# Optimization experiments

Measured on AMD Instinct MI355X. Metric: run time of the kernel, lower is better.

## Reference

```python
import jax, jax.numpy as jnp
import numpy as np

NUM_HEADS = 8
SCALE_BASE = 512.0
GN_EPS = 1e-5


def rotate_every_two(x):
    x1 = x[..., ::2]
    x2 = x[..., 1::2]
    return jnp.stack([-x2, x1], axis=-1).reshape(x.shape)


def xpos_apply(x, downscale):
    # x: [B, T, D]; XPOS rotary with length-dependent scale (offset=0)
    L, D = x.shape[1], x.shape[2]
    half = D // 2
    scale_vec = (jnp.arange(0, D, 2, dtype=jnp.float32) + 0.4 * D) / (1.4 * D)  # [half]
    pos = jnp.arange(L, dtype=jnp.float32)
    scale = scale_vec[None, :] ** (pos[:, None] / SCALE_BASE)  # [L, half]
    inv_freq = 1.0 / (10000.0 ** (jnp.arange(half, dtype=jnp.float32) / half))
    sinusoid = pos[:, None] * inv_freq[None, :]  # [L, half]
    sin, cos = jnp.sin(sinusoid), jnp.cos(sinusoid)
    if downscale:
        scale = 1.0 / scale
    sin_s = jnp.repeat(sin * scale, 2, axis=-1)  # duplicate_interleave -> [L, D]
    cos_s = jnp.repeat(cos * scale, 2, axis=-1)
    return x * cos_s + rotate_every_two(x) * sin_s


def decay_mask_fn(T, num_heads):
    # gamma per head; decay stored as log(gamma) so mask = gamma^(i-j) on lower triangle
    s, e = np.log(1.0 / 32.0), np.log(1.0 / 512.0)
    gamma = 1.0 - jnp.exp(jnp.linspace(s, e, num_heads).astype(jnp.float32))
    log_decay = jnp.log(gamma)  # [H], negative
    idx = jnp.arange(T)
    expo = (idx[:, None] - idx[None, :]).astype(jnp.float32)  # i - j
    tri = (idx[:, None] >= idx[None, :])
    expo_safe = jnp.where(tri, expo, 0.0)
    mask = jnp.exp(log_decay[:, None, None] * expo_safe) * tri  # [H, T, T]
    scale = jnp.sqrt(mask.sum(axis=-1, keepdims=True))  # [H, T, 1]
    return mask / scale


def setup_inputs() -> dict:
    key = jax.random.key(0)
    ks = jax.random.split(key, 4)
    B, T, E = 2, 2048, 1024
    V = 2 * E
    return {
        "hidden_states": jax.random.normal(ks[0], (B, T, E), dtype=jnp.float32),
        "w_qkv": jax.random.normal(ks[1], (E, 2 * E + V), dtype=jnp.float32) * 0.02,
        "b_qkv": jnp.zeros((2 * E + V,), dtype=jnp.float32),
        "w_g": jax.random.normal(ks[2], (E, V), dtype=jnp.float32) * 0.02,
        "b_g": jnp.zeros((V,), dtype=jnp.float32),
        "w_p": jax.random.normal(ks[3], (V, E), dtype=jnp.float32) * 0.02,
        "b_p": jnp.zeros((E,), dtype=jnp.float32),
    }


def reference(hidden_states, w_qkv, b_qkv, w_g, b_g, w_p, b_p):
    B, T, E = hidden_states.shape
    H = NUM_HEADS
    V = 2 * E
    dk, dv = E // H, V // H

    qkv = hidden_states @ w_qkv + b_qkv
    q, k, v = qkv[..., :E], qkv[..., E:2 * E], qkv[..., 2 * E:]
    q = xpos_apply(q, downscale=False)
    k = xpos_apply(k, downscale=True)

    # split heads -> [B, H, T, d]
    q = q.reshape(B, T, H, dk).transpose(0, 2, 1, 3)
    k = k.reshape(B, T, H, dk).transpose(0, 2, 1, 3)
    v = v.reshape(B, T, H, dv).transpose(0, 2, 1, 3)

    mask = decay_mask_fn(T, H)  # [H, T, T]

    # parallel retention
    retention = jnp.einsum("bhid,bhjd->bhij", q, k) * (dk ** -0.5)
    retention = retention * mask[None]  # [B, H, T, T]
    out = jnp.einsum("bhij,bhjv->bhiv", retention, v)

    # current_kv = sum_j mask[h, -1, j] * k_j (x) v_j
    curr_kv = jnp.einsum("hj,bhjk,bhjv->bhkv", mask[:, -1, :], k, v)

    retention_out = out.transpose(0, 2, 1, 3).reshape(B, T, V)

    # GroupNorm(num_groups=H, affine=False) over v_dim channels
    g = retention_out.reshape(B * T, H, dv)
    mu = g.mean(axis=-1, keepdims=True)
    var = ((g - mu) ** 2).mean(axis=-1, keepdims=True)
    normed = ((g - mu) / jnp.sqrt(var + GN_EPS)).reshape(B, T, V)

    gated = jax.nn.silu(hidden_states @ w_g + b_g) * normed
    proj = gated @ w_p + b_p
    return proj, curr_kv
```

## Files before the change

kernel.cpp:

```cpp
#include <hip/hip_runtime.h>
#include <math.h>

#define BT      4096
#define T_SEQ   2048
#define E_DIM   1024
#define V_DIM   2048
#define DK      128
#define DV      256

typedef unsigned short ushort_t;
typedef __attribute__((ext_vector_type(8)))  short bf16x8;
typedef __attribute__((ext_vector_type(4)))  unsigned short u16x4;
typedef __attribute__((ext_vector_type(16))) float f32x16;

__device__ __forceinline__ void decay_params(int h, float& ld, float& gamma) {
    const float s0 = -3.4657359027997265f;
    const float e0 = -6.2383246250395092f;
    float lin = s0 + (e0 - s0) * ((float)h * (1.0f / 7.0f));
    gamma = 1.0f - expf(lin);
    ld = logf(gamma);
}

__device__ __forceinline__ short f2bf(float f) {
    unsigned u = __float_as_uint(f);
    unsigned r = (u + 0x7fffu + ((u >> 16) & 1u)) >> 16;
    return (short)r;
}
__device__ __forceinline__ float bf2f(ushort_t u) {
    return __uint_as_float((unsigned)u << 16);
}

__device__ __forceinline__ void async_copy16(void* lds, const void* g) {
    __builtin_amdgcn_global_load_lds(
        (const __attribute__((address_space(1))) unsigned int*)g,
        (__attribute__((address_space(3))) unsigned int*)lds, 16, 0, 0);
}

__device__ __forceinline__ void xcd_tile(int& bx, int& by) {
    const int nwgx = gridDim.x;
    const int nwg  = nwgx * gridDim.y;
    int bid = blockIdx.y * nwgx + blockIdx.x;
    bid = (bid & 7) * (nwg >> 3) + (bid >> 3);
    bx = bid % nwgx;
    by = bid / nwgx;
}

__device__ __forceinline__ void xcd_map_qkv(int& bx, int& by) {
    int bid = blockIdx.y * 16 + blockIdx.x;
    const int xcd = bid & 7, idx = bid >> 3;
    bx = (xcd & 1) * 8 + (idx & 7);
    by = (xcd >> 1) * 4 + (idx >> 3);
}

__device__ __forceinline__ void xcd_map_gate(int& bx, int& by) {
    int bid = blockIdx.y * 8 + blockIdx.x;
    const int xcd = bid & 7, idx = bid >> 3;
    bx = (xcd & 1) * 4 + (idx & 3);
    by = (xcd >> 1) * 8 + (idx >> 2);
}

__global__ __launch_bounds__(256)
void f32_to_bf16_kernel(const float* __restrict__ in, ushort_t* __restrict__ out)
{
    int i = (blockIdx.x * 256 + threadIdx.x) * 8;
    float4 a = *(const float4*)&in[i];
    float4 b = *(const float4*)&in[i + 4];
    bf16x8 o;
    o[0] = f2bf(a.x); o[1] = f2bf(a.y); o[2] = f2bf(a.z); o[3] = f2bf(a.w);
    o[4] = f2bf(b.x); o[5] = f2bf(b.y); o[6] = f2bf(b.z); o[7] = f2bf(b.w);
    *(bf16x8*)&out[i] = o;
}

__global__ __launch_bounds__(256)
void transpose_w_kernel(const float* __restrict__ W, ushort_t* __restrict__ Wt,
                        int K, int N)
{
    __shared__ float tile[32][33];
    const int k0 = blockIdx.y * 32, n0 = blockIdx.x * 32;
    const int t = threadIdx.x;
    const int r = t >> 3, c = (t & 7) * 4;
    float4 v = *(const float4*)&W[(size_t)(k0 + r) * N + n0 + c];
    tile[r][c] = v.x; tile[r][c + 1] = v.y; tile[r][c + 2] = v.z; tile[r][c + 3] = v.w;
    __syncthreads();
    u16x4 o;
    o[0] = (ushort_t)f2bf(tile[c][r]);
    o[1] = (ushort_t)f2bf(tile[c + 1][r]);
    o[2] = (ushort_t)f2bf(tile[c + 2][r]);
    o[3] = (ushort_t)f2bf(tile[c + 3][r]);
    *(u16x4*)&Wt[(size_t)(n0 + r) * K + k0 + c] = o;
}

__global__ __launch_bounds__(512, 2)
void gemm256p8(const ushort_t* __restrict__ A,
               const ushort_t* __restrict__ Bt,
               const float* __restrict__ bias,
               ushort_t* __restrict__ C, int ldc, int nkt)
{
    __shared__ ushort_t As[2 * 16384];
    __shared__ ushort_t Bs[2 * 16384];

    const int tid = threadIdx.x;
    const int wid = tid >> 6, l = tid & 63;
    const int lc = l & 31, q = l >> 5;
    const int wr = wid >> 2, wc = wid & 3;
    int bx, by; xcd_map_qkv(bx, by);
    const int m0 = by * 256, n0 = bx * 256;

    const int sra = tid >> 3;
    const int spa = (tid & 7) ^ (sra & 7);
    const ushort_t* gA = A + (size_t)(m0 + sra) * 1024 + spa * 8;
    const int srb = tid >> 2;
    const int spb = (tid & 3) ^ ((srb >> 1) & 3);
    const ushort_t* gB = Bt + (size_t)(n0 + srb) * 1024 + spb * 8;
    const int da = tid * 8;

    int arow0 = (wr * 128 +  0 + lc) * 64;
    int arow1 = (wr * 128 + 32 + lc) * 64;
    int arow2 = (wr * 128 + 64 + lc) * 64;
    int arow3 = (wr * 128 + 96 + lc) * 64;
    int sk0 = ((0 * 2 + q) ^ (lc & 7)) * 8;
    int sk1 = ((1 * 2 + q) ^ (lc & 7)) * 8;
    int sk2 = ((2 * 2 + q) ^ (lc & 7)) * 8;
    int sk3 = ((3 * 2 + q) ^ (lc & 7)) * 8;
    int brow0 = (wc * 64 +  0 + lc) * 32;
    int brow1 = (wc * 64 + 32 + lc) * 32;
    int tk0 = ((0 + q) ^ ((lc >> 1) & 3)) * 8;
    int tk1 = ((2 + q) ^ ((lc >> 1) & 3)) * 8;
    int tk2 = 8192 + ((0 + q) ^ ((lc >> 1) & 3)) * 8;
    int tk3 = 8192 + ((2 + q) ^ ((lc >> 1) & 3)) * 8;

    f32x16 acc[4][2];
    #pragma unroll
    for (int mi = 0; mi < 4; ++mi)
        #pragma unroll
        for (int ni = 0; ni < 2; ++ni)
            #pragma unroll
            for (int e = 0; e < 16; ++e) acc[mi][ni][e] = 0.0f;

    async_copy16(&As[da],          gA);
    async_copy16(&As[8192 + da],   gA + 131072);
    async_copy16(&Bs[da],          gB);
    async_copy16(&Bs[4096 + da],   gB + 131072);
    async_copy16(&As[4096 + da],   gA + 65536);
    async_copy16(&As[12288 + da],  gA + 196608);
    async_copy16(&Bs[8192 + da],   gB + 32);
    async_copy16(&Bs[12288 + da],  gB + 131072 + 32);
    gA += 64; gB += 64;
    asm volatile("s_waitcnt vmcnt(0)" ::: "memory");
    __builtin_amdgcn_s_barrier();

    int cur = 0;
    for (int t = 0; t < nkt - 1; ++t) {
        const int cb = cur * 16384;
        const int nb = 16384 - cb;
        bf16x8 a00 = *(const bf16x8*)&As[cb + arow0 + sk0];
        bf16x8 a01 = *(const bf16x8*)&As[cb + arow0 + sk1];
        bf16x8 a10 = *(const bf16x8*)&As[cb + arow1 + sk0];
        bf16x8 a11 = *(const bf16x8*)&As[cb + arow1 + sk1];
        bf16x8 b00 = *(const bf16x8*)&Bs[cb + brow0 + tk0];
        bf16x8 b01 = *(const bf16x8*)&Bs[cb + brow0 + tk1];
        bf16x8 b10 = *(const bf16x8*)&Bs[cb + brow1 + tk0];
        bf16x8 b11 = *(const bf16x8*)&Bs[cb + brow1 + tk1];
        async_copy16(&As[nb + da],        gA);
        async_copy16(&As[nb + 8192 + da], gA + 131072);
        async_copy16(&Bs[nb + da],        gB);
        async_copy16(&Bs[nb + 4096 + da], gB + 131072);
        __builtin_amdgcn_s_barrier();
        asm volatile("s_waitcnt lgkmcnt(0)" ::: "memory");
        __builtin_amdgcn_s_setprio(1);
        acc[0][0] = __builtin_amdgcn_mfma_f32_32x32x16_bf16(a00, b00, acc[0][0], 0, 0, 0);
        acc[0][1] = __builtin_amdgcn_mfma_f32_32x32x16_bf16(a00, b10, acc[0][1], 0, 0, 0);
        acc[1][0] = __builtin_amdgcn_mfma_f32_32x32x16_bf16(a10, b00, acc[1][0], 0, 0, 0);
        acc[1][1] = __builtin_amdgcn_mfma_f32_32x32x16_bf16(a10, b10, acc[1][1], 0, 0, 0);
        acc[0][0] = __builtin_amdgcn_mfma_f32_32x32x16_bf16(a01, b01, acc[0][0], 0, 0, 0);
        acc[0][1] = __builtin_amdgcn_mfma_f32_32x32x16_bf16(a01, b11, acc[0][1], 0, 0, 0);
        acc[1][0] = __builtin_amdgcn_mfma_f32_32x32x16_bf16(a11, b01, acc[1][0], 0, 0, 0);
        acc[1][1] = __builtin_amdgcn_mfma_f32_32x32x16_bf16(a11, b11, acc[1][1], 0, 0, 0);
        __builtin_amdgcn_s_setprio(0);
        asm volatile("s_waitcnt vmcnt(6)" ::: "memory");
        __builtin_amdgcn_s_barrier();
        bf16x8 a20 = *(const bf16x8*)&As[cb + arow2 + sk0];
        bf16x8 a21 = *(const bf16x8*)&As[cb + arow2 + sk1];
        bf16x8 a30 = *(const bf16x8*)&As[cb + arow3 + sk0];
        bf16x8 a31 = *(const bf16x8*)&As[cb + arow3 + sk1];
        async_copy16(&As[nb + 4096 + da],  gA + 65536);
        async_copy16(&As[nb + 12288 + da], gA + 196608);
        __builtin_amdgcn_s_barrier();
        asm volatile("s_waitcnt lgkmcnt(0)" ::: "memory");
        __builtin_amdgcn_s_setprio(1);
        acc[2][0] = __builtin_amdgcn_mfma_f32_32x32x16_bf16(a20, b00, acc[2][0], 0, 0, 0);
        acc[2][1] = __builtin_amdgcn_mfma_f32_32x32x16_bf16(a20, b10, acc[2][1], 0, 0, 0);
        acc[3][0] = __builtin_amdgcn_mfma_f32_32x32x16_bf16(a30, b00, acc[3][0], 0, 0, 0);
        acc[3][1] = __builtin_amdgcn_mfma_f32_32x32x16_bf16(a30, b10, acc[3][1], 0, 0, 0);
        acc[2][0] = __builtin_amdgcn_mfma_f32_32x32x16_bf16(a21, b01, acc[2][0], 0, 0, 0);
        acc[2][1] = __builtin_amdgcn_mfma_f32_32x32x16_bf16(a21, b11, acc[2][1], 0, 0, 0);
        acc[3][0] = __builtin_amdgcn_mfma_f32_32x32x16_bf16(a31, b01, acc[3][0], 0, 0, 0);
        acc[3][1] = __builtin_amdgcn_mfma_f32_32x32x16_bf16(a31, b11, acc[3][1], 0, 0, 0);
        __builtin_amdgcn_s_setprio(0);
        asm volatile("s_waitcnt vmcnt(6)" ::: "memory");
        __builtin_amdgcn_s_barrier();
        bf16x8 a02 = *(const bf16x8*)&As[cb + arow0 + sk2];
        bf16x8 a03 = *(const bf16x8*)&As[cb + arow0 + sk3];
        bf16x8 a12 = *(const bf16x8*)&As[cb + arow1 + sk2];
        bf16x8 a13 = *(const bf16x8*)&As[cb + arow1 + sk3];
        bf16x8 b02 = *(const bf16x8*)&Bs[cb + brow0 + tk2];
        bf16x8 b03 = *(const bf16x8*)&Bs[cb + brow0 + tk3];
        bf16x8 b12 = *(const bf16x8*)&Bs[cb + brow1 + tk2];
        bf16x8 b13 = *(const bf16x8*)&Bs[cb + brow1 + tk3];
        async_copy16(&Bs[nb + 8192 + da],  gB + 32);
        async_copy16(&Bs[nb + 12288 + da], gB + 131072 + 32);
        gA += 64; gB += 64;
        __builtin_amdgcn_s_barrier();
        asm volatile("s_waitcnt lgkmcnt(0)" ::: "memory");
        __builtin_amdgcn_s_setprio(1);
        acc[0][0] = __builtin_amdgcn_mfma_f32_32x32x16_bf16(a02, b02, acc[0][0], 0, 0, 0);
        acc[0][1] = __builtin_amdgcn_mfma_f32_32x32x16_bf16(a02, b12, acc[0][1], 0, 0, 0);
        acc[1][0] = __builtin_amdgcn_mfma_f32_32x32x16_bf16(a12, b02, acc[1][0], 0, 0, 0);
        acc[1][1] = __builtin_amdgcn_mfma_f32_32x32x16_bf16(a12, b12, acc[1][1], 0, 0, 0);
        acc[0][0] = __builtin_amdgcn_mfma_f32_32x32x16_bf16(a03, b03, acc[0][0], 0, 0, 0);
        acc[0][1] = __builtin_amdgcn_mfma_f32_32x32x16_bf16(a03, b13, acc[0][1], 0, 0, 0);
        acc[1][0] = __builtin_amdgcn_mfma_f32_32x32x16_bf16(a13, b03, acc[1][0], 0, 0, 0);
        acc[1][1] = __builtin_amdgcn_mfma_f32_32x32x16_bf16(a13, b13, acc[1][1], 0, 0, 0);
        __builtin_amdgcn_s_setprio(0);
        __builtin_amdgcn_s_barrier();
        bf16x8 a22 = *(const bf16x8*)&As[cb + arow2 + sk2];
        bf16x8 a23 = *(const bf16x8*)&As[cb + arow2 + sk3];
        bf16x8 a32 = *(const bf16x8*)&As[cb + arow3 + sk2];
        bf16x8 a33 = *(const bf16x8*)&As[cb + arow3 + sk3];
        __builtin_amdgcn_s_barrier();
        asm volatile("s_waitcnt lgkmcnt(0)" ::: "memory");
        __builtin_amdgcn_s_setprio(1);
        acc[2][0] = __builtin_amdgcn_mfma_f32_32x32x16_bf16(a22, b02, acc[2][0], 0, 0, 0);
        acc[2][1] = __builtin_amdgcn_mfma_f32_32x32x16_bf16(a22, b12, acc[2][1], 0, 0, 0);
        acc[3][0] = __builtin_amdgcn_mfma_f32_32x32x16_bf16(a32, b02, acc[3][0], 0, 0, 0);
        acc[3][1] = __builtin_amdgcn_mfma_f32_32x32x16_bf16(a32, b12, acc[3][1], 0, 0, 0);
        acc[2][0] = __builtin_amdgcn_mfma_f32_32x32x16_bf16(a23, b03, acc[2][0], 0, 0, 0);
        acc[2][1] = __builtin_amdgcn_mfma_f32_32x32x16_bf16(a23, b13, acc[2][1], 0, 0, 0);
        acc[3][0] = __builtin_amdgcn_mfma_f32_32x32x16_bf16(a33, b03, acc[3][0], 0, 0, 0);
        acc[3][1] = __builtin_amdgcn_mfma_f32_32x32x16_bf16(a33, b13, acc[3][1], 0, 0, 0);
        __builtin_amdgcn_s_setprio(0);
        asm volatile("s_waitcnt vmcnt(4)" ::: "memory");
        __builtin_amdgcn_s_barrier();
        cur ^= 1;
    }

    {
        const int cb = cur * 16384;
        bf16x8 a00 = *(const bf16x8*)&As[cb + arow0 + sk0];
        bf16x8 a01 = *(const bf16x8*)&As[cb + arow0 + sk1];
        bf16x8 a10 = *(const bf16x8*)&As[cb + arow1 + sk0];
        bf16x8 a11 = *(const bf16x8*)&As[cb + arow1 + sk1];
        bf16x8 b00 = *(const bf16x8*)&Bs[cb + brow0 + tk0];
        bf16x8 b01 = *(const bf16x8*)&Bs[cb + brow0 + tk1];
        bf16x8 b10 = *(const bf16x8*)&Bs[cb + brow1 + tk0];
        bf16x8 b11 = *(const bf16x8*)&Bs[cb + brow1 + tk1];
        __builtin_amdgcn_s_barrier();
        asm volatile("s_waitcnt lgkmcnt(0)" ::: "memory");
        __builtin_amdgcn_s_setprio(1);
        acc[0][0] = __builtin_amdgcn_mfma_f32_32x32x16_bf16(a00, b00, acc[0][0], 0, 0, 0);
        acc[0][1] = __builtin_amdgcn_mfma_f32_32x32x16_bf16(a00, b10, acc[0][1], 0, 0, 0);
        acc[1][0] = __builtin_amdgcn_mfma_f32_32x32x16_bf16(a10, b00, acc[1][0], 0, 0, 0);
        acc[1][1] = __builtin_amdgcn_mfma_f32_32x32x16_bf16(a10, b10, acc[1][1], 0, 0, 0);
        acc[0][0] = __builtin_amdgcn_mfma_f32_32x32x16_bf16(a01, b01, acc[0][0], 0, 0, 0);
        acc[0][1] = __builtin_amdgcn_mfma_f32_32x32x16_bf16(a01, b11, acc[0][1], 0, 0, 0);
        acc[1][0] = __builtin_amdgcn_mfma_f32_32x32x16_bf16(a11, b01, acc[1][0], 0, 0, 0);
        acc[1][1] = __builtin_amdgcn_mfma_f32_32x32x16_bf16(a11, b11, acc[1][1], 0, 0, 0);
        __builtin_amdgcn_s_setprio(0);
        asm volatile("s_waitcnt vmcnt(2)" ::: "memory");
        __builtin_amdgcn_s_barrier();
        bf16x8 a20 = *(const bf16x8*)&As[cb + arow2 + sk0];
        bf16x8 a21 = *(const bf16x8*)&As[cb + arow2 + sk1];
        bf16x8 a30 = *(const bf16x8*)&As[cb + arow3 + sk0];
        bf16x8 a31 = *(const bf16x8*)&As[cb + arow3 + sk1];
        __builtin_amdgcn_s_barrier();
        asm volatile("s_waitcnt lgkmcnt(0)" ::: "memory");
        __builtin_amdgcn_s_setprio(1);
        acc[2][0] = __builtin_amdgcn_mfma_f32_32x32x16_bf16(a20, b00, acc[2][0], 0, 0, 0);
        acc[2][1] = __builtin_amdgcn_mfma_f32_32x32x16_bf16(a20, b10, acc[2][1], 0, 0, 0);
        acc[3][0] = __builtin_amdgcn_mfma_f32_32x32x16_bf16(a30, b00, acc[3][0], 0, 0, 0);
        acc[3][1] = __builtin_amdgcn_mfma_f32_32x32x16_bf16(a30, b10, acc[3][1], 0, 0, 0);
        acc[2][0] = __builtin_amdgcn_mfma_f32_32x32x16_bf16(a21, b01, acc[2][0], 0, 0, 0);
        acc[2][1] = __builtin_amdgcn_mfma_f32_32x32x16_bf16(a21, b11, acc[2][1], 0, 0, 0);
        acc[3][0] = __builtin_amdgcn_mfma_f32_32x32x16_bf16(a31, b01, acc[3][0], 0, 0, 0);
        acc[3][1] = __builtin_amdgcn_mfma_f32_32x32x16_bf16(a31, b11, acc[3][1], 0, 0, 0);
        __builtin_amdgcn_s_setprio(0);
        asm volatile("s_waitcnt vmcnt(0)" ::: "memory");
        __builtin_amdgcn_s_barrier();
        bf16x8 a02 = *(const bf16x8*)&As[cb + arow0 + sk2];
        bf16x8 a03 = *(const bf16x8*)&As[cb + arow0 + sk3];
        bf16x8 a12 = *(const bf16x8*)&As[cb + arow1 + sk2];
        bf16x8 a13 = *(const bf16x8*)&As[cb + arow1 + sk3];
        bf16x8 b02 = *(const bf16x8*)&Bs[cb + brow0 + tk2];
        bf16x8 b03 = *(const bf16x8*)&Bs[cb + brow0 + tk3];
        bf16x8 b12 = *(const bf16x8*)&Bs[cb + brow1 + tk2];
        bf16x8 b13 = *(const bf16x8*)&Bs[cb + brow1 + tk3];
        __builtin_amdgcn_s_barrier();
        asm volatile("s_waitcnt lgkmcnt(0)" ::: "memory");
        __builtin_amdgcn_s_setprio(1);
        acc[0][0] = __builtin_amdgcn_mfma_f32_32x32x16_bf16(a02, b02, acc[0][0], 0, 0, 0);
        acc[0][1] = __builtin_amdgcn_mfma_f32_32x32x16_bf16(a02, b12, acc[0][1], 0, 0, 0);
        acc[1][0] = __builtin_amdgcn_mfma_f32_32x32x16_bf16(a12, b02, acc[1][0], 0, 0, 0);
        acc[1][1] = __builtin_amdgcn_mfma_f32_32x32x16_bf16(a12, b12, acc[1][1], 0, 0, 0);
        acc[0][0] = __builtin_amdgcn_mfma_f32_32x32x16_bf16(a03, b03, acc[0][0], 0, 0, 0);
        acc[0][1] = __builtin_amdgcn_mfma_f32_32x32x16_bf16(a03, b13, acc[0][1], 0, 0, 0);
        acc[1][0] = __builtin_amdgcn_mfma_f32_32x32x16_bf16(a13, b03, acc[1][0], 0, 0, 0);
        acc[1][1] = __builtin_amdgcn_mfma_f32_32x32x16_bf16(a13, b13, acc[1][1], 0, 0, 0);
        __builtin_amdgcn_s_setprio(0);
        __builtin_amdgcn_s_barrier();
        bf16x8 a22 = *(const bf16x8*)&As[cb + arow2 + sk2];
        bf16x8 a23 = *(const bf16x8*)&As[cb + arow2 + sk3];
        bf16x8 a32 = *(const bf16x8*)&As[cb + arow3 + sk2];
        bf16x8 a33 = *(const bf16x8*)&As[cb + arow3 + sk3];
        asm volatile("s_waitcnt lgkmcnt(0)" ::: "memory");
        __builtin_amdgcn_s_setprio(1);
        acc[2][0] = __builtin_amdgcn_mfma_f32_32x32x16_bf16(a22, b02, acc[2][0], 0, 0, 0);
        acc[2][1] = __builtin_amdgcn_mfma_f32_32x32x16_bf16(a22, b12, acc[2][1], 0, 0, 0);
        acc[3][0] = __builtin_amdgcn_mfma_f32_32x32x16_bf16(a32, b02, acc[3][0], 0, 0, 0);
        acc[3][1] = __builtin_amdgcn_mfma_f32_32x32x16_bf16(a32, b12, acc[3][1], 0, 0, 0);
        acc[2][0] = __builtin_amdgcn_mfma_f32_32x32x16_bf16(a23, b03, acc[2][0], 0, 0, 0);
        acc[2][1] = __builtin_amdgcn_mfma_f32_32x32x16_bf16(a23, b13, acc[2][1], 0, 0, 0);
        acc[3][0] = __builtin_amdgcn_mfma_f32_32x32x16_bf16(a33, b03, acc[3][0], 0, 0, 0);
        acc[3][1] = __builtin_amdgcn_mfma_f32_32x32x16_bf16(a33, b13, acc[3][1], 0, 0, 0);
        __builtin_amdgcn_s_setprio(0);
    }

    {
        const float bb0 = bias[n0 + wc * 64 + lc];
        const float bb1 = bias[n0 + wc * 64 + 32 + lc];
        #pragma unroll
        for (int mi = 0; mi < 4; ++mi) {
            #pragma unroll
            for (int r = 0; r < 16; ++r) {
                const int row = m0 + wr * 128 + mi * 32 + (r & 3) + 8 * (r >> 2) + 4 * q;
                ushort_t* cp = C + (size_t)row * ldc + n0 + wc * 64 + lc;
                cp[0]  = (ushort_t)f2bf(acc[mi][0][r] + bb0);
                cp[32] = (ushort_t)f2bf(acc[mi][1][r] + bb1);
            }
        }
    }
}

__global__ __launch_bounds__(512)
void gemm_gate_p8(const ushort_t* __restrict__ A,
                  const ushort_t* __restrict__ Bt,
                  const float* __restrict__ bias,
                  ushort_t* __restrict__ C, int ldc,
                  int nkt)
{
    __shared__ ushort_t As[2 * 8192];
    __shared__ ushort_t Bs[2 * 16384];

    const int tid = threadIdx.x;
    const int wid = tid >> 6, l = tid & 63;
    const int lc = l & 31, q = l >> 5;
    const int wr = wid >> 2, wc = wid & 3;
    int bx, by; xcd_map_gate(bx, by);
    const int m0 = by * 128, n0 = bx * 256;

    const int sra = tid >> 3;
    const int spa = (tid & 7) ^ (sra & 7);
    const ushort_t* gA = A + (size_t)(m0 + sra) * 1024 + spa * 8;
    const int srb = tid >> 2;
    const int spb = (tid & 3) ^ ((srb >> 1) & 3);
    const ushort_t* gB = Bt + (size_t)(n0 + srb) * 1024 + spb * 8;
    const int da = tid * 8;

    int arow0 = (wr * 64 +  0 + lc) * 64;
    int arow1 = (wr * 64 + 32 + lc) * 64;
    int sk0 = ((0 * 2 + q) ^ (lc & 7)) * 8;
    int sk1 = ((1 * 2 + q) ^ (lc & 7)) * 8;
    int sk2 = ((2 * 2 + q) ^ (lc & 7)) * 8;
    int sk3 = ((3 * 2 + q) ^ (lc & 7)) * 8;
    int brow0 = (wc * 64 +  0 + lc) * 32;
    int brow1 = (wc * 64 + 32 + lc) * 32;
    int tk0 = ((0 + q) ^ ((lc >> 1) & 3)) * 8;
    int tk1 = ((2 + q) ^ ((lc >> 1) & 3)) * 8;
    int tk2 = 8192 + ((0 + q) ^ ((lc >> 1) & 3)) * 8;
    int tk3 = 8192 + ((2 + q) ^ ((lc >> 1) & 3)) * 8;

    f32x16 acc[2][2];
    #pragma unroll
    for (int mi = 0; mi < 2; ++mi)
        #pragma unroll
        for (int ni = 0; ni < 2; ++ni)
            #pragma unroll
            for (int e = 0; e < 16; ++e) acc[mi][ni][e] = 0.0f;

    async_copy16(&As[da],          gA);
    async_copy16(&As[4096 + da],   gA + 65536);
    async_copy16(&Bs[da],          gB);
    async_copy16(&Bs[4096 + da],   gB + 131072);
    async_copy16(&Bs[8192 + da],   gB + 32);
    async_copy16(&Bs[12288 + da],  gB + 131072 + 32);
    gA += 64; gB += 64;
    asm volatile("s_waitcnt vmcnt(0)" ::: "memory");
    __builtin_amdgcn_s_barrier();

    int cur = 0;
    for (int t = 0; t < nkt - 1; ++t) {
        const int ca = cur * 8192,  na = 8192 - ca;
        const int cb = cur * 16384, nb = 16384 - cb;
        bf16x8 a00 = *(const bf16x8*)&As[ca + arow0 + sk0];
        bf16x8 a01 = *(const bf16x8*)&As[ca + arow0 + sk1];
        bf16x8 a10 = *(const bf16x8*)&As[ca + arow1 + sk0];
        bf16x8 a11 = *(const bf16x8*)&As[ca + arow1 + sk1];
        bf16x8 b00 = *(const bf16x8*)&Bs[cb + brow0 + tk0];
        bf16x8 b01 = *(const bf16x8*)&Bs[cb + brow0 + tk1];
        bf16x8 b10 = *(const bf16x8*)&Bs[cb + brow1 + tk0];
        bf16x8 b11 = *(const bf16x8*)&Bs[cb + brow1 + tk1];
        async_copy16(&As[na + da],        gA);
        async_copy16(&As[na + 4096 + da], gA + 65536);
        async_copy16(&Bs[nb + da],        gB);
        async_copy16(&Bs[nb + 4096 + da], gB + 131072);
        __builtin_amdgcn_s_barrier();
        asm volatile("s_waitcnt lgkmcnt(0)" ::: "memory");
        __builtin_amdgcn_s_setprio(1);
        acc[0][0] = __builtin_amdgcn_mfma_f32_32x32x16_bf16(a00, b00, acc[0][0], 0, 0, 0);
// ... 442 lines not shown
            pa1[e]     = f2bf(q ? t3 : sv[e + 8]);
            pa1[e + 4] = f2bf(q ? sv[e + 12] : t2);
        }

        #pragma unroll
        for (int vg = 0; vg < 8; ++vg) {
            const ushort_t* vp = vt + ((size_t)bh * 256 + vg * 32 + lc) * T_SEQ + j0 + q * 8;
            bf16x8 vb0 = *(const bf16x8*)vp;
            bf16x8 vb1 = *(const bf16x8*)(vp + 16);
            acc[vg] = __builtin_amdgcn_mfma_f32_32x32x16_bf16(pa0, vb0, acc[vg], 0, 0, 0);
            acc[vg] = __builtin_amdgcn_mfma_f32_32x32x16_bf16(pa1, vb1, acc[vg], 0, 0, 0);
        }
    }

    #pragma unroll
    for (int r = 0; r < 16; ++r) {
        const int il = (r & 3) + 8 * (r >> 2) + 4 * q;
        const int i  = i0 + il;
        float denom = (1.0f - expf(ld * (float)(i + 1))) / (1.0f - gamma);
        float fs = 0.08838834764831845f * rsqrtf(denom);
        float vals[8];
        float a1 = 0.0f, a2 = 0.0f;
        #pragma unroll
        for (int vg = 0; vg < 8; ++vg) {
            float x = acc[vg][r] * fs;
            vals[vg] = x;
            a1 += x; a2 += x * x;
        }
        a1 += __shfl_xor(a1, 1);  a2 += __shfl_xor(a2, 1);
        a1 += __shfl_xor(a1, 2);  a2 += __shfl_xor(a2, 2);
        a1 += __shfl_xor(a1, 4);  a2 += __shfl_xor(a2, 4);
        a1 += __shfl_xor(a1, 8);  a2 += __shfl_xor(a2, 8);
        a1 += __shfl_xor(a1, 16); a2 += __shfl_xor(a2, 16);
        float mu = a1 * (1.0f / 256.0f);
        float var = a2 * (1.0f / 256.0f) - mu * mu;
        float rs = rsqrtf(var + 1e-5f);
        const size_t ob = ((size_t)(b * T_SEQ + i)) * V_DIM + h * DV + lc;
        ushort_t* op = gated + ob;
        const ushort_t* gp = grw + ob;
        #pragma unroll
        for (int vg = 0; vg < 8; ++vg) {
            float g = bf2f(gp[vg * 32]);
            op[vg * 32] = (ushort_t)f2bf((vals[vg] - mu) * rs * g);
        }
    }
}

extern "C" void kernel_launch(void* const* d_in, const int* in_sizes, int n_in,
                              void* d_out, int out_size, void* d_ws, size_t ws_size,
                              hipStream_t stream)
{
    const float* hs    = (const float*)d_in[0];
    const float* w_qkv = (const float*)d_in[1];
    const float* b_qkv = (const float*)d_in[2];
    const float* w_g   = (const float*)d_in[3];
    const float* b_g   = (const float*)d_in[4];
    const float* w_p   = (const float*)d_in[5];
    const float* b_p   = (const float*)d_in[6];
    float* out = (float*)d_out;

    const size_t MB = 1024 * 1024;
    ushort_t* qkv_bf   = (ushort_t*)d_ws;
    ushort_t* Abuf     = (ushort_t*)d_ws;
    ushort_t* Stbuf    = (ushort_t*)d_ws;
    ushort_t* wp_t     = (ushort_t*)d_ws;
    ushort_t* gate_raw = (ushort_t*)((char*)d_ws + 32 * MB);
    ushort_t* gated_bf = (ushort_t*)((char*)d_ws + 48 * MB);
    ushort_t* wg_t     = (ushort_t*)((char*)d_ws + 64 * MB);
    ushort_t* qh       = (ushort_t*)((char*)d_ws + 64 * MB);
    ushort_t* vt       = (ushort_t*)((char*)d_ws + 72 * MB);
    ushort_t* wqkv_t   = (ushort_t*)((char*)d_ws + 88 * MB);
    ushort_t* kh       = (ushort_t*)((char*)d_ws + 88 * MB);
    ushort_t* hs_bf    = (ushort_t*)d_out;
    ushort_t* kt2      = (ushort_t*)((char*)d_out + 8 * MB);
    float*    ckv_out  = out + (size_t)BT * E_DIM;

    f32_to_bf16_kernel<<<dim3(2048), 256, 0, stream>>>(hs, hs_bf);
    transpose_w_kernel<<<dim3(64, 32), 256, 0, stream>>>(w_g, wg_t, E_DIM, V_DIM);
    transpose_w_kernel<<<dim3(128, 32), 256, 0, stream>>>(w_qkv, wqkv_t, E_DIM, 4096);

    gemm_gate_p8<<<dim3(8, 32), 512, 0, stream>>>(
        hs_bf, wg_t, b_g, gate_raw, V_DIM, E_DIM / 64);

    gemm256p8<<<dim3(16, 16), 512, 0, stream>>>(
        hs_bf, wqkv_t, b_qkv, qkv_bf, 4096, E_DIM / 64);

    qk_prep<<<dim3(BT), 256, 0, stream>>>(qkv_bf, qh, kh);
    v_transpose<<<dim3(64, 128), 256, 0, stream>>>(qkv_bf, vt);
    kt2_kernel<<<dim3(64, 64), 256, 0, stream>>>(kh, kt2);

    chunk_kv<<<dim3(32, 16), 256, 0, stream>>>(vt, kt2, Abuf);
    scan_state<<<dim3(2048), 256, 0, stream>>>(Abuf, Stbuf, ckv_out);
    retention_chunk<<<dim3(64, 16), 64, 0, stream>>>(qh, kh, vt, Stbuf, gate_raw, gated_bf);

    transpose_w_kernel<<<dim3(32, 64), 256, 0, stream>>>(w_p, wp_t, V_DIM, E_DIM);
    gemm_tm64<<<dim3(8, 64), 256, 0, stream>>>(
        gated_bf, V_DIM, wp_t, V_DIM, b_p, out, E_DIM, V_DIM / 32);
}
```

Before: 297.4 us.

## Rewrite QKV GEMM as 256x128 tile with 3-stage BK=32 LDS pipeline

```diff
diff --git a/kernel.cpp b/kernel.cpp
--- a/kernel.cpp
+++ b/kernel.cpp
@@ -45,11 +45,11 @@
     by = bid / nwgx;
 }
 
-__device__ __forceinline__ void xcd_map_qkv(int& bx, int& by) {
-    int bid = blockIdx.y * 16 + blockIdx.x;
+__device__ __forceinline__ void xcd_map_qkv2(int& bx, int& by) {
+    int bid = blockIdx.y * 32 + blockIdx.x;
     const int xcd = bid & 7, idx = bid >> 3;
-    bx = (xcd & 1) * 8 + (idx & 7);
-    by = (xcd >> 1) * 4 + (idx >> 3);
+    bx = (xcd & 3) * 8 + (idx & 7);
+    by = (xcd >> 2) * 8 + (idx >> 3);
 }
 
 __device__ __forceinline__ void xcd_map_gate(int& bx, int& by) {
@@ -90,44 +90,40 @@
     *(u16x4*)&Wt[(size_t)(n0 + r) * K + k0 + c] = o;
 }
 
-__global__ __launch_bounds__(512, 2)
-void gemm256p8(const ushort_t* __restrict__ A,
-               const ushort_t* __restrict__ Bt,
-               const float* __restrict__ bias,
-               ushort_t* __restrict__ C, int ldc, int nkt)
-{
-    __shared__ ushort_t As[2 * 16384];
-    __shared__ ushort_t Bs[2 * 16384];
+__global__ __launch_bounds__(256, 2)
+void gemm_qkv_v2(const ushort_t* __restrict__ A,
+                 const ushort_t* __restrict__ Bt,
+                 const float* __restrict__ bias,
+                 ushort_t* __restrict__ C, int ldc, int nkt)
+{
+    __shared__ ushort_t As[3 * 8192];
+    __shared__ ushort_t Bs[3 * 4096];
 
     const int tid = threadIdx.x;
-    const int wid = tid >> 6, l = tid & 63;
+    const int w  = tid >> 6, l = tid & 63;
     const int lc = l & 31, q = l >> 5;
-    const int wr = wid >> 2, wc = wid & 3;
-    int bx, by; xcd_map_qkv(bx, by);
-    const int m0 = by * 256, n0 = bx * 256;
-
-    const int sra = tid >> 3;
-    const int spa = (tid & 7) ^ (sra & 7);
-    const ushort_t* gA = A + (size_t)(m0 + sra) * 1024 + spa * 8;
-    const int srb = tid >> 2;
-    const int spb = (tid & 3) ^ ((srb >> 1) & 3);
-    const ushort_t* gB = Bt + (size_t)(n0 + srb) * 1024 + spb * 8;
-    const int da = tid * 8;
-
-    int arow0 = (wr * 128 +  0 + lc) * 64;
-    int arow1 = (wr * 128 + 32 + lc) * 64;
-    int arow2 = (wr * 128 + 64 + lc) * 64;
-    int arow3 = (wr * 128 + 96 + lc) * 64;
-    int sk0 = ((0 * 2 + q) ^ (lc & 7)) * 8;
-    int sk1 = ((1 * 2 + q) ^ (lc & 7)) * 8;
-    int sk2 = ((2 * 2 + q) ^ (lc & 7)) * 8;
-    int sk3 = ((3 * 2 + q) ^ (lc & 7)) * 8;
-    int brow0 = (wc * 64 +  0 + lc) * 32;
-    int brow1 = (wc * 64 + 32 + lc) * 32;
-    int tk0 = ((0 + q) ^ ((lc >> 1) & 3)) * 8;
-    int tk1 = ((2 + q) ^ ((lc >> 1) & 3)) * 8;
-    int tk2 = 8192 + ((0 + q) ^ ((lc >> 1) & 3)) * 8;
-    int tk3 = 8192 + ((2 + q) ^ ((lc >> 1) & 3)) * 8;
+    const int wr = w >> 1, wcn = w & 1;
+    int bx, by; xcd_map_qkv2(bx, by);
+    const int m0 = by * 256, n0 = bx * 128;
+
+    const int rb = tid >> 2;
+    const int kc = (tid & 3) ^ ((rb >> 1) & 3);
+    const ushort_t* gA = A  + (size_t)(m0 + rb) * 1024 + kc * 8;
+    const ushort_t* gB = Bt + (size_t)(n0 + rb) * 1024 + kc * 8;
+    const int dst = tid * 8;
+
+    const int sl = (lc >> 1) & 3;
+    int aoff[4][2], boff[2][2];
+    #pragma unroll
+    for (int ks = 0; ks < 2; ++ks) {
+        const int kk = ks * 2 + q;
+        #pragma unroll
+        for (int mi = 0; mi < 4; ++mi)
+            aoff[mi][ks] = ((wr * 128 + mi * 32 + lc) * 4 + (kk ^ sl)) * 8;
+        #pragma unroll
+        for (int ni = 0; ni < 2; ++ni)
+            boff[ni][ks] = ((wcn * 64 + ni * 32 + lc) * 4 + (kk ^ sl)) * 8;
+    }
 
     f32x16 acc[4][2];
     #pragma unroll
@@ -137,34 +133,36 @@
             #pragma unroll
             for (int e = 0; e < 16; ++e) acc[mi][ni][e] = 0.0f;
 
-    async_copy16(&As[da],          gA);
-    async_copy16(&As[8192 + da],   gA + 131072);
-    async_copy16(&Bs[da],          gB);
-    async_copy16(&Bs[4096 + da],   gB + 131072);
-    async_copy16(&As[4096 + da],   gA + 65536);
-    async_copy16(&As[12288 + da],  gA + 196608);
-    async_copy16(&Bs[8192 + da],   gB + 32);
-    async_copy16(&Bs[12288 + da],  gB + 131072 + 32);
-    gA += 64; gB += 64;
-    asm volatile("s_waitcnt vmcnt(0)" ::: "memory");
+    auto stageA = [&](int ab) {
+        async_copy16(&As[ab + 0 * 2048 + dst], gA + 0 * 65536);
+        async_copy16(&As[ab + 1 * 2048 + dst], gA + 1 * 65536);
+        async_copy16(&As[ab + 2 * 2048 + dst], gA + 2 * 65536);
+        async_copy16(&As[ab + 3 * 2048 + dst], gA + 3 * 65536);
+        gA += 32;
+    };
+    auto stageB = [&](int bb) {
+        async_copy16(&Bs[bb + 0 * 2048 + dst], gB + 0 * 65536);
+        async_copy16(&Bs[bb + 1 * 2048 + dst], gB + 1 * 65536);
+        gB += 32;
+    };
+
+    stageA(0);     stageB(0);
+    stageA(8192);  stageB(4096);
+    asm volatile("s_waitcnt vmcnt(6)" ::: "memory");
     __builtin_amdgcn_s_barrier();
 
-    int cur = 0;
-    for (int t = 0; t < nkt - 1; ++t) {
-        const int cb = cur * 16384;
-        const int nb = 16384 - cb;
-        bf16x8 a00 = *(const bf16x8*)&As[cb + arow0 + sk0];
-        bf16x8 a01 = *(const bf16x8*)&As[cb + arow0 + sk1];
-        bf16x8 a10 = *(const bf16x8*)&As[cb + arow1 + sk0];
-        bf16x8 a11 = *(const bf16x8*)&As[cb + arow1 + sk1];
-        bf16x8 b00 = *(const bf16x8*)&Bs[cb + brow0 + tk0];
-        bf16x8 b01 = *(const bf16x8*)&Bs[cb + brow0 + tk1];
-        bf16x8 b10 = *(const bf16x8*)&Bs[cb + brow1 + tk0];
-        bf16x8 b11 = *(const bf16x8*)&Bs[cb + brow1 + tk1];
-        async_copy16(&As[nb + da],        gA);
-        async_copy16(&As[nb + 8192 + da], gA + 131072);
-        async_copy16(&Bs[nb + da],        gB);
-        async_copy16(&Bs[nb + 4096 + da], gB + 131072);
+    int as_ = 16384, bs_ = 8192;
+    int ac_ = 0,     bc_ = 0;
+    for (int t = 0; t < nkt - 2; ++t) {
+        bf16x8 b00 = *(const bf16x8*)&Bs[bc_ + boff[0][0]];
+        bf16x8 b01 = *(const bf16x8*)&Bs[bc_ + boff[0][1]];
+        bf16x8 b10 = *(const bf16x8*)&Bs[bc_ + boff[1][0]];
+        bf16x8 b11 = *(const bf16x8*)&Bs[bc_ + boff[1][1]];
+        bf16x8 a00 = *(const bf16x8*)&As[ac_ + aoff[0][0]];
+        bf16x8 a01 = *(const bf16x8*)&As[ac_ + aoff[0][1]];
+        bf16x8 a10 = *(const bf16x8*)&As[ac_ + aoff[1][0]];
+        bf16x8 a11 = *(const bf16x8*)&As[ac_ + aoff[1][1]];
+        stageA(as_);
         __builtin_amdgcn_s_barrier();
         asm volatile("s_waitcnt lgkmcnt(0)" ::: "memory");
         __builtin_amdgcn_s_setprio(1);
@@ -177,14 +175,12 @@
         acc[1][0] = __builtin_amdgcn_mfma_f32_32x32x16_bf16(a11, b01, acc[1][0], 0, 0, 0);
         acc[1][1] = __builtin_amdgcn_mfma_f32_32x32x16_bf16(a11, b11, acc[1][1], 0, 0, 0);
         __builtin_amdgcn_s_setprio(0);
-        asm volatile("s_waitcnt vmcnt(6)" ::: "memory");
-        __builtin_amdgcn_s_barrier();
-        bf16x8 a20 = *(const bf16x8*)&As[cb + arow2 + sk0];
-        bf16x8 a21 = *(const bf16x8*)&As[cb + arow2 + sk1];
-        bf16x8 a30 = *(const bf16x8*)&As[cb + arow3 + sk0];
-        bf16x8 a31 = *(const bf16x8*)&As[cb + arow3 + sk1];
-        async_copy16(&As[nb + 4096 + da],  gA + 65536);
-        async_copy16(&As[nb + 12288 + da], gA + 196608);
+        __builtin_amdgcn_s_barrier();
+        bf16x8 a20 = *(const bf16x8*)&As[ac_ + aoff[2][0]];
+        bf16x8 a21 = *(const bf16x8*)&As[ac_ + aoff[2][1]];
+        bf16x8 a30 = *(const bf16x8*)&As[ac_ + aoff[3][0]];
+        bf16x8 a31 = *(const bf16x8*)&As[ac_ + aoff[3][1]];
+        stageB(bs_);
         __builtin_amdgcn_s_barrier();
         asm volatile("s_waitcnt lgkmcnt(0)" ::: "memory");
         __builtin_amdgcn_s_setprio(1);
@@ -199,140 +195,64 @@
         __builtin_amdgcn_s_setprio(0);
         asm volatile("s_waitcnt vmcnt(6)" ::: "memory");
         __builtin_amdgcn_s_barrier();
-        bf16x8 a02 = *(const bf16x8*)&As[cb + arow0 + sk2];
-        bf16x8 a03 = *(const bf16x8*)&As[cb + arow0 + sk3];
-        bf16x8 a12 = *(const bf16x8*)&As[cb + arow1 + sk2];
-        bf16x8 a13 = *(const bf16x8*)&As[cb + arow1 + sk3];
-        bf16x8 b02 = *(const bf16x8*)&Bs[cb + brow0 + tk2];
-        bf16x8 b03 = *(const bf16x8*)&Bs[cb + brow0 + tk3];
-        bf16x8 b12 = *(const bf16x8*)&Bs[cb + brow1 + tk2];
-        bf16x8 b13 = *(const bf16x8*)&Bs[cb + brow1 + tk3];
-        async_copy16(&Bs[nb + 8192 + da],  gB + 32);
-        async_copy16(&Bs[nb + 12288 + da], gB + 131072 + 32);
-        gA += 64; gB += 64;
-        __builtin_amdgcn_s_barrier();
-        asm volatile("s_waitcnt lgkmcnt(0)" ::: "memory");
-        __builtin_amdgcn_s_setprio(1);
-        acc[0][0] = __builtin_amdgcn_mfma_f32_32x32x16_bf16(a02, b02, acc[0][0], 0, 0, 0);
-        acc[0][1] = __builtin_amdgcn_mfma_f32_32x32x16_bf16(a02, b12, acc[0][1], 0, 0, 0);
-        acc[1][0] = __builtin_amdgcn_mfma_f32_32x32x16_bf16(a12, b02, acc[1][0], 0, 0, 0);
-        acc[1][1] = __builtin_amdgcn_mfma_f32_32x32x16_bf16(a12, b12, acc[1][1], 0, 0, 0);
-        acc[0][0] = __builtin_amdgcn_mfma_f32_32x32x16_bf16(a03, b03, acc[0][0], 0, 0, 0);
-        acc[0][1] = __builtin_amdgcn_mfma_f32_32x32x16_bf16(a03, b13, acc[0][1], 0, 0, 0);
-        acc[1][0] = __builtin_amdgcn_mfma_f32_32x32x16_bf16(a13, b03, acc[1][0], 0, 0, 0);
-        acc[1][1] = __builtin_amdgcn_mfma_f32_32x32x16_bf16(a13, b13, acc[1][1], 0, 0, 0);
-        __builtin_amdgcn_s_setprio(0);
-        __builtin_amdgcn_s_barrier();
-        bf16x8 a22 = *(const bf16x8*)&As[cb + arow2 + sk2];
-        bf16x8 a23 = *(const bf16x8*)&As[cb + arow2 + sk3];
-        bf16x8 a32 = *(const bf16x8*)&As[cb + arow3 + sk2];
-        bf16x8 a33 = *(const bf16x8*)&As[cb + arow3 + sk3];
-        __builtin_amdgcn_s_barrier();
-        asm volatile("s_waitcnt lgkmcnt(0)" ::: "memory");
-        __builtin_amdgcn_s_setprio(1);
-        acc[2][0] = __builtin_amdgcn_mfma_f32_32x32x16_bf16(a22, b02, acc[2][0], 0, 0, 0);
-        acc[2][1] = __builtin_amdgcn_mfma_f32_32x32x16_bf16(a22, b12, acc[2][1], 0, 0, 0);
-        acc[3][0] = __builtin_amdgcn_mfma_f32_32x32x16_bf16(a32, b02, acc[3][0], 0, 0, 0);
-        acc[3][1] = __builtin_amdgcn_mfma_f32_32x32x16_bf16(a32, b12, acc[3][1], 0, 0, 0);
-        acc[2][0] = __builtin_amdgcn_mfma_f32_32x32x16_bf16(a23, b03, acc[2][0], 0, 0, 0);
-        acc[2][1] = __builtin_amdgcn_mfma_f32_32x32x16_bf16(a23, b13, acc[2][1], 0, 0, 0);
-        acc[3][0] = __builtin_amdgcn_mfma_f32_32x32x16_bf16(a33, b03, acc[3][0], 0, 0, 0);
-        acc[3][1] = __builtin_amdgcn_mfma_f32_32x32x16_bf16(a33, b13, acc[3][1], 0, 0, 0);
-        __builtin_amdgcn_s_setprio(0);
-        asm volatile("s_waitcnt vmcnt(4)" ::: "memory");
-        __builtin_amdgcn_s_barrier();
-        cur ^= 1;
+        as_ = ac_; bs_ = bc_;
+        ac_ = (ac_ == 16384) ? 0 : ac_ + 8192;
+        bc_ = (bc_ == 8192)  ? 0 : bc_ + 4096;
     }
 
     {
-        const int cb = cur * 16384;
-        bf16x8 a00 = *(const bf16x8*)&As[cb + arow0 + sk0];
-        bf16x8 a01 = *(const bf16x8*)&As[cb + arow0 + sk1];
-        bf16x8 a10 = *(const bf16x8*)&As[cb + arow1 + sk0];
-        bf16x8 a11 = *(const bf16x8*)&As[cb + arow1 + sk1];
-        bf16x8 b00 = *(const bf16x8*)&Bs[cb + brow0 + tk0];
-        bf16x8 b01 = *(const bf16x8*)&Bs[cb + brow0 + tk1];
-        bf16x8 b10 = *(const bf16x8*)&Bs[cb + brow1 + tk0];
-        bf16x8 b11 = *(const bf16x8*)&Bs[cb + brow1 + tk1];
-        __builtin_amdgcn_s_barrier();
-        asm volatile("s_waitcnt lgkmcnt(0)" ::: "memory");
-        __builtin_amdgcn_s_setprio(1);
-        acc[0][0] = __builtin_amdgcn_mfma_f32_32x32x16_bf16(a00, b00, acc[0][0], 0, 0, 0);
-        acc[0][1] = __builtin_amdgcn_mfma_f32_32x32x16_bf16(a00, b10, acc[0][1], 0, 0, 0);
-        acc[1][0] = __builtin_amdgcn_mfma_f32_32x32x16_bf16(a10, b00, acc[1][0], 0, 0, 0);
-        acc[1][1] = __builtin_amdgcn_mfma_f32_32x32x16_bf16(a10, b10, acc[1][1], 0, 0, 0);
-        acc[0][0] = __builtin_amdgcn_mfma_f32_32x32x16_bf16(a01, b01, acc[0][0], 0, 0, 0);
-        acc[0][1] = __builtin_amdgcn_mfma_f32_32x32x16_bf16(a01, b11, acc[0][1], 0, 0, 0);
-        acc[1][0] = __builtin_amdgcn_mfma_f32_32x32x16_bf16(a11, b01, acc[1][0], 0, 0, 0);
-        acc[1][1] = __builtin_amdgcn_mfma_f32_32x32x16_bf16(a11, b11, acc[1][1], 0, 0, 0);
-        __builtin_amdgcn_s_setprio(0);
-        asm volatile("s_waitcnt vmcnt(2)" ::: "memory");
-        __builtin_amdgcn_s_barrier();
-        bf16x8 a20 = *(const bf16x8*)&As[cb + arow2 + sk0];
-        bf16x8 a21 = *(const bf16x8*)&As[cb + arow2 + sk1];
-        bf16x8 a30 = *(const bf16x8*)&As[cb + arow3 + sk0];
-        bf16x8 a31 = *(const bf16x8*)&As[cb + arow3 + sk1];
-        __builtin_amdgcn_s_barrier();
-        asm volatile("s_waitcnt lgkmcnt(0)" ::: "memory");
-        __builtin_amdgcn_s_setprio(1);
-        acc[2][0] = __builtin_amdgcn_mfma_f32_32x32x16_bf16(a20, b00, acc[2][0], 0, 0, 0);
-        acc[2][1] = __builtin_amdgcn_mfma_f32_32x32x16_bf16(a20, b10, acc[2][1], 0, 0, 0);
-        acc[3][0] = __builtin_amdgcn_mfma_f32_32x32x16_bf16(a30, b00, acc[3][0], 0, 0, 0);
-        acc[3][1] = __builtin_amdgcn_mfma_f32_32x32x16_bf16(a30, b10, acc[3][1], 0, 0, 0);
-        acc[2][0] = __builtin_amdgcn_mfma_f32_32x32x16_bf16(a21, b01, acc[2][0], 0, 0, 0);
-        acc[2][1] = __builtin_amdgcn_mfma_f32_32x32x16_bf16(a21, b11, acc[2][1], 0, 0, 0);
-        acc[3][0] = __builtin_amdgcn_mfma_f32_32x32x16_bf16(a31, b01, acc[3][0], 0, 0, 0);
-        acc[3][1] = __builtin_amdgcn_mfma_f32_32x32x16_bf16(a31, b11, acc[3][1], 0, 0, 0);
-        __builtin_amdgcn_s_setprio(0);
+        bf16x8 b00 = *(const bf16x8*)&Bs[bc_ + boff[0][0]];
+        bf16x8 b01 = *(const bf16x8*)&Bs[bc_ + boff[0][1]];
+        bf16x8 b10 = *(const bf16x8*)&Bs[bc_ + boff[1][0]];
+        bf16x8 b11 = *(const bf16x8*)&Bs[bc_ + boff[1][1]];
+        #pragma unroll
+        for (int mp = 0; mp < 2; ++mp) {
+            bf16x8 x00 = *(const bf16x8*)&As[ac_ + aoff[mp * 2 + 0][0]];
+            bf16x8 x01 = *(const bf16x8*)&As[ac_ + aoff[mp * 2 + 0][1]];
+            bf16x8 x10 = *(const bf16x8*)&As[ac_ + aoff[mp * 2 + 1][0]];
+            bf16x8 x11 = *(const bf16x8*)&As[ac_ + aoff[mp * 2 + 1][1]];
+            asm volatile("s_waitcnt lgkmcnt(0)" ::: "memory");
+            __builtin_amdgcn_s_setprio(1);
+            acc[mp*2+0][0] = __builtin_amdgcn_mfma_f32_32x32x16_bf16(x00, b00, acc[mp*2+0][0], 0, 0, 0);
+            acc[mp*2+0][1] = __builtin_amdgcn_mfma_f32_32x32x16_bf16(x00, b10, acc[mp*2+0][1], 0, 0, 0);
+            acc[mp*2+1][0] = __builtin_amdgcn_mfma_f32_32x32x16_bf16(x10, b00, acc[mp*2+1][0], 0, 0, 0);
+            acc[mp*2+1][1] = __builtin_amdgcn_mfma_f32_32x32x16_bf16(x10, b10, acc[mp*2+1][1], 0, 0, 0);
+            acc[mp*2+0][0] = __builtin_amdgcn_mfma_f32_32x32x16_bf16(x01, b01, acc[mp*2+0][0], 0, 0, 0);
+            acc[mp*2+0][1] = __builtin_amdgcn_mfma_f32_32x32x16_bf16(x01, b11, acc[mp*2+0][1], 0, 0, 0);
+            acc[mp*2+1][0] = __builtin_amdgcn_mfma_f32_32x32x16_bf16(x11, b01, acc[mp*2+1][0], 0, 0, 0);
+            acc[mp*2+1][1] = __builtin_amdgcn_mfma_f32_32x32x16_bf16(x11, b11, acc[mp*2+1][1], 0, 0, 0);
+            __builtin_amdgcn_s_setprio(0);
+        }
         asm volatile("s_waitcnt vmcnt(0)" ::: "memory");
         __builtin_amdgcn_s_barrier();
-        bf16x8 a02 = *(const bf16x8*)&As[cb + arow0 + sk2];
-        bf16x8 a03 = *(const bf16x8*)&As[cb + arow0 + sk3];
-        bf16x8 a12 = *(const bf16x8*)&As[cb + arow1 + sk2];
-        bf16x8 a13 = *(const bf16x8*)&As[cb + arow1 + sk3];
-        bf16x8 b02 = *(const bf16x8*)&Bs[cb + brow0 + tk2];
-        bf16x8 b03 = *(const bf16x8*)&Bs[cb + brow0 + tk3];
-        bf16x8 b12 = *(const bf16x8*)&Bs[cb + brow1 + tk2];
-        bf16x8 b13 = *(const bf16x8*)&Bs[cb + brow1 + tk3];
-        __builtin_amdgcn_s_barrier();
-        asm volatile("s_waitcnt lgkmcnt(0)" ::: "memory");
-        __builtin_amdgcn_s_setprio(1);
-        acc[0][0] = __builtin_amdgcn_mfma_f32_32x32x16_bf16(a02, b02, acc[0][0], 0, 0, 0);
-        acc[0][1] = __builtin_amdgcn_mfma_f32_32x32x16_bf16(a02, b12, acc[0][1], 0, 0, 0);
-        acc[1][0] = __builtin_amdgcn_mfma_f32_32x32x16_bf16(a12, b02, acc[1][0], 0, 0, 0);
-        acc[1][1] = __builtin_amdgcn_mfma_f32_32x32x16_bf16(a12, b12, acc[1][1], 0, 0, 0);
-        acc[0][0] = __builtin_amdgcn_mfma_f32_32x32x16_bf16(a03, b03, acc[0][0], 0, 0, 0);
-        acc[0][1] = __builtin_amdgcn_mfma_f32_32x32x16_bf16(a03, b13, acc[0][1], 0, 0, 0);
-        acc[1][0] = __builtin_amdgcn_mfma_f32_32x32x16_bf16(a13, b03, acc[1][0], 0, 0, 0);
-        acc[1][1] = __builtin_amdgcn_mfma_f32_32x32x16_bf16(a13, b13, acc[1][1], 0, 0, 0);
-        __builtin_amdgcn_s_setprio(0);
-        __builtin_amdgcn_s_barrier();
-        bf16x8 a22 = *(const bf16x8*)&As[cb + arow2 + sk2];
-        bf16x8 a23 = *(const bf16x8*)&As[cb + arow2 + sk3];
-        bf16x8 a32 = *(const bf16x8*)&As[cb + arow3 + sk2];
-        bf16x8 a33 = *(const bf16x8*)&As[cb + arow3 + sk3];
-        asm volatile("s_waitcnt lgkmcnt(0)" ::: "memory");
-        __builtin_amdgcn_s_setprio(1);
-        acc[2][0] = __builtin_amdgcn_mfma_f32_32x32x16_bf16(a22, b02, acc[2][0], 0, 0, 0);
-        acc[2][1] = __builtin_amdgcn_mfma_f32_32x32x16_bf16(a22, b12, acc[2][1], 0, 0, 0);
-        acc[3][0] = __builtin_amdgcn_mfma_f32_32x32x16_bf16(a32, b02, acc[3][0], 0, 0, 0);
-        acc[3][1] = __builtin_amdgcn_mfma_f32_32x32x16_bf16(a32, b12, acc[3][1], 0, 0, 0);
-        acc[2][0] = __builtin_amdgcn_mfma_f32_32x32x16_bf16(a23, b03, acc[2][0], 0, 0, 0);
-        acc[2][1] = __builtin_amdgcn_mfma_f32_32x32x16_bf16(a23, b13, acc[2][1], 0, 0, 0);
-        acc[3][0] = __builtin_amdgcn_mfma_f32_32x32x16_bf16(a33, b03, acc[3][0], 0, 0, 0);
-        acc[3][1] = __builtin_amdgcn_mfma_f32_32x32x16_bf16(a33, b13, acc[3][1], 0, 0, 0);
-        __builtin_amdgcn_s_setprio(0);
-    }
-
+        ac_ = (ac_ == 16384) ? 0 : ac_ + 8192;
+        bc_ = (bc_ == 8192)  ? 0 : bc_ + 4096;
+    }
     {
-        const float bb0 = bias[n0 + wc * 64 + lc];
-        const float bb1 = bias[n0 + wc * 64 + 32 + lc];
+        bf16x8 b00 = *(const bf16x8*)&Bs[bc_ + boff[0][0]];
+        bf16x8 b01 = *(const bf16x8*)&Bs[bc_ + boff[0][1]];
+        bf16x8 b10 = *(const bf16x8*)&Bs[bc_ + boff[1][0]];
+        bf16x8 b11 = *(const bf16x8*)&Bs[bc_ + boff[1][1]];
+        #pragma unroll
+        for (int mi = 0; mi < 4; ++mi) {
+            bf16x8 x0 = *(const bf16x8*)&As[ac_ + aoff[mi][0]];
+            bf16x8 x1 = *(const bf16x8*)&As[ac_ + aoff[mi][1]];
+            acc[mi][0] = __builtin_amdgcn_mfma_f32_32x32x16_bf16(x0, b00, acc[mi][0], 0, 0, 0);
+            acc[mi][1] = __builtin_amdgcn_mfma_f32_32x32x16_bf16(x0, b10, acc[mi][1], 0, 0, 0);
+            acc[mi][0] = __builtin_amdgcn_mfma_f32_32x32x16_bf16(x1, b01, acc[mi][0], 0, 0, 0);
+            acc[mi][1] = __builtin_amdgcn_mfma_f32_32x32x16_bf16(x1, b11, acc[mi][1], 0, 0, 0);
+        }
+    }
+
+    {
+        const float bb0 = bias[n0 + wcn * 64 + lc];
+        const float bb1 = bias[n0 + wcn * 64 + 32 + lc];
         #pragma unroll
         for (int mi = 0; mi < 4; ++mi) {
             #pragma unroll
             for (int r = 0; r < 16; ++r) {
                 const int row = m0 + wr * 128 + mi * 32 + (r & 3) + 8 * (r >> 2) + 4 * q;
-                ushort_t* cp = C + (size_t)row * ldc + n0 + wc * 64 + lc;
+                ushort_t* cp = C + (size_t)row * ldc + n0 + wcn * 64 + lc;
                 cp[0]  = (ushort_t)f2bf(acc[mi][0][r] + bb0);
                 cp[32] = (ushort_t)f2bf(acc[mi][1][r] + bb1);
             }
@@ -941,8 +861,8 @@
     gemm_gate_p8<<<dim3(8, 32), 512, 0, stream>>>(
         hs_bf, wg_t, b_g, gate_raw, V_DIM, E_DIM / 64);
 
-    gemm256p8<<<dim3(16, 16), 512, 0, stream>>>(
-        hs_bf, wqkv_t, b_qkv, qkv_bf, 4096, E_DIM / 64);
+    gemm_qkv_v2<<<dim3(32, 16), 256, 0, stream>>>(
+        hs_bf, wqkv_t, b_qkv, qkv_bf, 4096, E_DIM / 32);
 
     qk_prep<<<dim3(BT), 256, 0, stream>>>(qkv_bf, qh, kh);
     v_transpose<<<dim3(64, 128), 256, 0, stream>>>(qkv_bf, vt);
```

Result: no change. 297.1 us (-0.1%).
